# Performance work log

Measured on AMD Instinct MI355X. Metric: run time of the kernel, lower is better.

The kernel has to match this reference:

```python
import jax, jax.numpy as jnp
import numpy as np

B, N, C_FEAT = 2, 1024, 64
S, K, K_FP = 512, 32, 3
D_MODEL, N_HEAD = 128, 4
EPS_BN = 1e-5


def square_distance(src, dst):
    # src [B,N,3], dst [B,M,3] -> [B,N,M], same expansion as torch version
    d = -2.0 * jnp.einsum('bnc,bmc->bnm', src, dst)
    d = d + jnp.sum(src ** 2, -1)[:, :, None]
    d = d + jnp.sum(dst ** 2, -1)[:, None, :]
    return d


def gather_points(points, idx):
    # points [B,N,C], idx [B,...] int -> [B,...,C]  (index_points)
    return jax.vmap(lambda p, i: p[i])(points, idx)


def fps(xyz, n_samples):
    # furthest point sampling, deterministic start at index 0
    Bs, Np, _ = xyz.shape
    def step(carry, _):
        dist, far = carry
        centroid = jax.vmap(lambda p, i: p[i])(xyz, far)  # [B,3]
        d = jnp.sum((xyz - centroid[:, None, :]) ** 2, -1)
        dist = jnp.minimum(dist, d)
        new_far = jnp.argmax(dist, -1).astype(jnp.int32)
        return (dist, new_far), far
    init = (jnp.full((Bs, Np), 1e10, xyz.dtype), jnp.zeros((Bs,), jnp.int32))
    _, idxs = jax.lax.scan(step, init, None, length=n_samples)
    return idxs.T  # [B,S]


def knn(nsample, xyz, new_xyz):
    d = square_distance(new_xyz, xyz)
    _, idx = jax.lax.top_k(-d, nsample)
    return idx  # [B, n_query, nsample]


def setup_inputs() -> dict:
    key = jax.random.key(0)
    ks = jax.random.split(key, 12)
    Din = 2 * C_FEAT + 3  # 131 = 3 + 2*channels (PreExtraction in_channels)
    def lin(k, fan_in, shape):
        return (jax.random.normal(k, shape, jnp.float32) / np.sqrt(fan_in)).astype(jnp.float32)
    z = lambda n: jnp.zeros((n,), jnp.float32)
    return {
        'xyz': jax.random.normal(ks[0], (B, N, 3), jnp.float32),
        'feats': jax.random.normal(ks[1], (B, N, C_FEAT), jnp.float32),
        'affine_alpha': jnp.ones((1, 1, 1, C_FEAT + 3), jnp.float32),
        'affine_beta': jnp.zeros((1, 1, 1, C_FEAT + 3), jnp.float32),
        'W_t': lin(ks[2], Din, (Din, D_MODEL)), 'b_t': z(D_MODEL),
        'bn_g': jnp.ones((D_MODEL,), jnp.float32), 'bn_b': z(D_MODEL),
        'Wq': lin(ks[3], D_MODEL, (D_MODEL, D_MODEL)), 'bq': z(D_MODEL),
        'Wk': lin(ks[4], D_MODEL, (D_MODEL, D_MODEL)), 'bk': z(D_MODEL),
        'Wv': lin(ks[5], D_MODEL, (D_MODEL, D_MODEL)), 'bv': z(D_MODEL),
        'Wo': lin(ks[6], D_MODEL, (D_MODEL, D_MODEL)), 'bo': z(D_MODEL),
        'Wp1': lin(ks[7], 3, (3, D_MODEL)), 'bp1': z(D_MODEL),
        'Wp2': lin(ks[8], D_MODEL, (D_MODEL, N_HEAD)), 'bp2': z(N_HEAD),
    }


def reference(xyz, feats, affine_alpha, affine_beta, W_t, b_t, bn_g, bn_b,
              Wq, bq, Wk, bk, Wv, bv, Wo, bo, Wp1, bp1, Wp2, bp2):
    # ---- LocalGrouper (FPS + KNN + gather + center-normalize + affine) ----
    fps_idx = fps(xyz, S)                       # [B,S]
    new_xyz = gather_points(xyz, fps_idx)       # [B,S,3]
    anchor_feats = gather_points(feats, fps_idx)  # [B,S,C]
    idx = knn(K, xyz, new_xyz)                  # [B,S,K]
    grouped_xyz = gather_points(xyz, idx)       # [B,S,K,3]
    grouped_pts = gather_points(feats, idx)     # [B,S,K,C]
    grouped = jnp.concatenate([grouped_pts, grouped_xyz], -1)  # [B,S,K,C+3]
    mean = jnp.mean(grouped, axis=2, keepdims=True)
    std = jnp.std((grouped - mean).reshape(B, -1), axis=-1, ddof=1)[:, None, None, None]
    grouped = (grouped - mean) / (std + 1e-5)
    grouped = affine_alpha * grouped + affine_beta
    anchor_rep = jnp.broadcast_to(anchor_feats[:, :, None, :], (B, S, K, C_FEAT))
    new_points = jnp.concatenate([grouped, anchor_rep], -1)  # [B,S,K,2C+3]
    # ---- PreExtraction transfer (1x1 conv + BN(eval) + ReLU) + max over K ----
    y = jnp.einsum('bskd,do->bsko', new_points, W_t) + b_t
    y = y * (bn_g / jnp.sqrt(1.0 + EPS_BN)) + bn_b  # BN with running stats (0,1)
    y = jax.nn.relu(y)
    v_k = jnp.max(y, axis=2)                    # [B,S,D_MODEL]
    # ---- PointNetFeaturePropagation (KNN-3 inverse-distance interp) ----
    idx_fp = knn(K_FP, new_xyz, xyz)            # [B,N,3]
    sqrd = square_distance(xyz, new_xyz)        # [B,N,S]
    d_near = jnp.clip(jnp.take_along_axis(sqrd, idx_fp, axis=2), 1e-10, None)
    w = 1.0 / d_near
    w = w / jnp.sum(w, -1, keepdims=True)
    grouped_v = gather_points(v_k, idx_fp)      # [B,N,3,D]
    v_q = jnp.einsum('bnk,bnkc->bnc', w, grouped_v)  # [B,N,D]
    # ---- PointTransformerCrossAttention ----
    Dh = D_MODEL // N_HEAD
    qh = (v_q @ Wq + bq).reshape(B, N, N_HEAD, Dh)
    kh = (v_k @ Wk + bk).reshape(B, S, N_HEAD, Dh)
    vh = (v_k @ Wv + bv).reshape(B, S, N_HEAD, Dh)
    rel = xyz[:, :, None, :] - new_xyz[:, None, :, :]         # [B,N,S,3]
    rpe = jax.nn.relu(rel @ Wp1 + bp1) @ Wp2 + bp2            # [B,N,S,H]
    energy = jnp.einsum('bihd,bjhd->bhij', qh, kh) / jnp.sqrt(jnp.float32(Dh))
    attn = jax.nn.softmax(energy + rpe.transpose(0, 3, 1, 2), axis=-1)
    out = jnp.einsum('bhij,bjhd->bihd', attn, vh).reshape(B, N, D_MODEL)
    return out @ Wo + bo
```

## Files before the change

### kernel.cpp

```cpp
#include <hip/hip_runtime.h>
#include <math.h>

namespace {

constexpr int B  = 2;
constexpr int N  = 1024;
constexpr int CF = 64;
constexpr int S  = 512;
constexpr int K  = 32;
constexpr int DM = 128;
constexpr int NH = 4;
constexpr int DH = 32;
constexpr int GC = 67;
constexpr int DIN = 131;
constexpr int DPAD = 132;
constexpr int EPAD = 516;

typedef float f2 __attribute__((ext_vector_type(2)));

__device__ inline float max3f(float a, float b, float c) { return fmaxf(fmaxf(a, b), c); }
__device__ inline unsigned min3u(unsigned a, unsigned b, unsigned c) { return min(min(a, b), c); }

template <int CTRL>
__device__ inline float dpp_mov_f(float v) {
  return __int_as_float(__builtin_amdgcn_update_dpp(0, __float_as_int(v), CTRL, 0xF, 0xF, true));
}
template <int CTRL>
__device__ inline unsigned dpp_mov_self_u(unsigned v) {
  return (unsigned)__builtin_amdgcn_update_dpp((int)v, (int)v, CTRL, 0xF, 0xF, false);
}

__global__ void __launch_bounds__(64, 1)
fps_kernel(const float* __restrict__ xyz, int* __restrict__ fps_idx,
           float* __restrict__ new_xyz) {
  const int b = blockIdx.x;
  const int lane = threadIdx.x;
  __shared__ __align__(16) float4 pts4[N];
  __shared__ int farhist[S];
  for (int p = lane; p < N; p += 64) {
    pts4[p] = make_float4(xyz[b*N*3 + p*3+0], xyz[b*N*3 + p*3+1], xyz[b*N*3 + p*3+2], 0.0f);
  }
  __syncthreads();
  f2 X[8], Y[8], Z[8];
  float dist[16];
  #pragma unroll
  for (int j = 0; j < 8; ++j) {
    const float4 a = pts4[(2*j)*64 + lane];
    const float4 c = pts4[(2*j+1)*64 + lane];
    X[j] = f2{a.x, c.x}; Y[j] = f2{a.y, c.y}; Z[j] = f2{a.z, c.z};
  }
  #pragma unroll
  for (int k = 0; k < 16; ++k) dist[k] = 1e10f;
  int far = 0;
  for (int s = 0; s < S; ++s) {
    if (lane == 0) farhist[s] = far;
    const float4 c = pts4[far];
    const f2 cx = f2{c.x, c.x}, cy = f2{c.y, c.y}, cz = f2{c.z, c.z};
    #pragma unroll
    for (int j = 0; j < 8; ++j) {
      const f2 dx = X[j] - cx, dy = Y[j] - cy, dz = Z[j] - cz;
      const f2 q = dx*dx + dy*dy + dz*dz;
      dist[2*j]   = fminf(dist[2*j],   q.x);
      dist[2*j+1] = fminf(dist[2*j+1], q.y);
    }
    const float l0 = max3f(dist[0],  dist[1],  dist[2]);
    const float l1 = max3f(dist[3],  dist[4],  dist[5]);
    const float l2 = max3f(dist[6],  dist[7],  dist[8]);
    const float l3 = max3f(dist[9],  dist[10], dist[11]);
    const float l4 = max3f(dist[12], dist[13], dist[14]);
    float mv = fmaxf(max3f(l0, l1, l2), max3f(l3, l4, dist[15]));
    mv = fmaxf(mv, dpp_mov_f<0x111>(mv));
    mv = fmaxf(mv, dpp_mov_f<0x112>(mv));
    mv = fmaxf(mv, dpp_mov_f<0x114>(mv));
    mv = fmaxf(mv, dpp_mov_f<0x118>(mv));
    mv = fmaxf(mv, dpp_mov_f<0x142>(mv));
    mv = fmaxf(mv, dpp_mov_f<0x143>(mv));
    const float maxv = __int_as_float(__builtin_amdgcn_readlane(__float_as_int(mv), 63));
    unsigned cnd[16];
    #pragma unroll
    for (int k = 0; k < 16; ++k) {
      cnd[k] = (dist[k] == maxv) ? (unsigned)(k*64 + lane) : 0xFFFFFFFFu;
    }
    const unsigned u0 = min3u(cnd[0],  cnd[1],  cnd[2]);
    const unsigned u1 = min3u(cnd[3],  cnd[4],  cnd[5]);
    const unsigned u2 = min3u(cnd[6],  cnd[7],  cnd[8]);
    const unsigned u3 = min3u(cnd[9],  cnd[10], cnd[11]);
    const unsigned u4 = min3u(cnd[12], cnd[13], cnd[14]);
    unsigned cand = min(min3u(u0, u1, u2), min3u(u3, u4, cnd[15]));
    cand = min(cand, dpp_mov_self_u<0x111>(cand));
    cand = min(cand, dpp_mov_self_u<0x112>(cand));
    cand = min(cand, dpp_mov_self_u<0x114>(cand));
    cand = min(cand, dpp_mov_self_u<0x118>(cand));
    cand = min(cand, dpp_mov_self_u<0x142>(cand));
    cand = min(cand, dpp_mov_self_u<0x143>(cand));
    far = __builtin_amdgcn_readlane((int)cand, 63);
  }
  __syncthreads();
  for (int s = lane; s < S; s += 64) {
    const int f = farhist[s];
    const float4 c = pts4[f];
    fps_idx[b*S+s] = f;
    new_xyz[(b*S+s)*3+0] = c.x;
    new_xyz[(b*S+s)*3+1] = c.y;
    new_xyz[(b*S+s)*3+2] = c.z;
  }
}

__global__ void knn_kernel(const float* __restrict__ xyz, const float* __restrict__ feats,
                           const float* __restrict__ new_xyz, int* __restrict__ knn_idx,
                           float* __restrict__ mean_out, float2* __restrict__ partials) {
  const int b = blockIdx.y;
  const int tid = threadIdx.x;
  const int wave = tid >> 6, lane = tid & 63;
  const int s = blockIdx.x * 4 + wave;
  __shared__ float pts[N*3];
  __shared__ int sidx_s[4][K];
  for (int i = tid; i < N*3; i += 256) pts[i] = xyz[b*N*3 + i];
  __syncthreads();
  const float qx = new_xyz[(b*S+s)*3+0], qy = new_xyz[(b*S+s)*3+1], qz = new_xyz[(b*S+s)*3+2];
  const float qn = qx*qx + qy*qy + qz*qz;
  float d[16];
  #pragma unroll
  for (int j = 0; j < 16; ++j) {
    const int p = j*64 + lane;
    const float px = pts[p*3+0], py = pts[p*3+1], pz = pts[p*3+2];
    const float dot = qx*px + qy*py + qz*pz;
    const float pn  = px*px + py*py + pz*pz;
    d[j] = (-2.0f*dot + qn) + pn;
  }
  unsigned mask = 0xFFFFu;
  for (int k = 0; k < K; ++k) {
    float bv = INFINITY; int bj = 0;
    #pragma unroll
    for (int j = 0; j < 16; ++j) {
      if (((mask >> j) & 1u) && d[j] < bv) { bv = d[j]; bj = j; }
    }
    int bp = bj*64 + lane;
    #pragma unroll
    for (int m = 1; m < 64; m <<= 1) {
      const float ov = __shfl_xor(bv, m);
      const int   op = __shfl_xor(bp, m);
      if (ov < bv || (ov == bv && op < bp)) { bv = ov; bp = op; }
    }
    if (lane == 0) { knn_idx[(b*S+s)*K + k] = bp; sidx_s[wave][k] = bp; }
    if ((bp & 63) == lane) mask &= ~(1u << (bp >> 6));
  }
  const int bs = b*S + s;
  float ls = 0.0f, lsq = 0.0f;
  float v[K];
  {
    const int c = lane;
    float sum = 0.0f;
    #pragma unroll
    for (int k = 0; k < K; ++k) {
      const int p = sidx_s[wave][k];
      const float g = feats[(b*N+p)*CF + c];
      v[k] = g; sum += g;
    }
    const float mean = sum * (1.0f/K);
    mean_out[bs*GC + c] = mean;
    #pragma unroll
    for (int k = 0; k < K; ++k) {
      const float cc = v[k] - mean;
      ls += cc; lsq += cc*cc;
    }
  }
  if (lane < 3) {
    const int c = CF + lane;
    float sum = 0.0f;
    #pragma unroll
    for (int k = 0; k < K; ++k) {
      const int p = sidx_s[wave][k];
      const float g = xyz[(b*N+p)*3 + lane];
      v[k] = g; sum += g;
    }
    const float mean = sum * (1.0f/K);
    mean_out[bs*GC + c] = mean;
    #pragma unroll
    for (int k = 0; k < K; ++k) {
      const float cc = v[k] - mean;
      ls += cc; lsq += cc*cc;
    }
  }
  #pragma unroll
  for (int m = 1; m < 64; m <<= 1) { ls += __shfl_xor(ls, m); lsq += __shfl_xor(lsq, m); }
  if (lane == 0) partials[bs] = make_float2(ls, lsq);
}

__global__ void stats_kernel(const float2* __restrict__ partials, float* __restrict__ invstd) {
  const int b = blockIdx.x;
  const int lane = threadIdx.x;
  double su = 0.0, sq = 0.0;
  for (int i = lane; i < S; i += 64) {
    const float2 p = partials[b*S+i];
    su += (double)p.x; sq += (double)p.y;
  }
  #pragma unroll
  for (int m = 1; m < 64; m <<= 1) { su += __shfl_xor(su, m); sq += __shfl_xor(sq, m); }
  if (lane == 0) {
    const double nn = (double)S * K * GC;
    const double var = (sq - su*su/nn) / (nn - 1.0);
    invstd[b] = 1.0f / ((float)sqrt(var) + 1e-5f);
  }
}

__global__ void transfer_kernel(const float* __restrict__ feats, const float* __restrict__ xyz,
                                const int* __restrict__ knn_idx, const int* __restrict__ fps_idx,
                                const float* __restrict__ mean_in, const float* __restrict__ invstd,
                                const float* __restrict__ alpha, const float* __restrict__ beta,
                                const float* __restrict__ W_t, const float* __restrict__ b_t,
                                const float* __restrict__ bn_g, const float* __restrict__ bn_b,
                                const float* __restrict__ Wk, const float* __restrict__ bk,
                                const float* __restrict__ Wv, const float* __restrict__ bv,
                                float* __restrict__ v_k, float* __restrict__ kpb,
                                float* __restrict__ vpb) {
  const int bs = blockIdx.x;
  const int b = bs / S;
  const int t = threadIdx.x;
  __shared__ __align__(16) float np_s[K][DPAD];
  __shared__ float vrow[DM];
  __shared__ int sidx[K];
  __shared__ int sanchor;
  if (t < K) sidx[t] = knn_idx[bs*K + t];
  if (t == 0) sanchor = fps_idx[bs];
  __syncthreads();
  const float sinv = invstd[b];
  for (int k = 0; k < K; ++k) {
    const int p = sidx[k];
    for (int c = t; c < DPAD; c += 128) {
      float val = 0.0f;
      if (c < GC) {
        const float g = (c < CF) ? feats[(b*N+p)*CF + c] : xyz[(b*N+p)*3 + (c-CF)];
        val = (g - mean_in[bs*GC + c]) * sinv * alpha[c] + beta[c];
      } else if (c < DIN) {
        val = feats[(b*N+sanchor)*CF + (c - GC)];
      }
      np_s[k][c] = val;
    }
  }
  __syncthreads();
  float acc[K];
  const float bt = b_t[t];
  #pragma unroll
  for (int k = 0; k < K; ++k) acc[k] = bt;
  for (int d4 = 0; d4 < DPAD/4; ++d4) {
    const int d = d4*4;
    const float w0 = W_t[(d+0)*DM + t];
    const float w1 = W_t[(d+1)*DM + t];
    const float w2 = W_t[(d+2)*DM + t];
    const float w3 = (d+3 < DIN) ? W_t[(d+3)*DM + t] : 0.0f;
    #pragma unroll
    for (int k = 0; k < K; ++k) {
      const float4 f = *reinterpret_cast<const float4*>(&np_s[k][d]);
      acc[k] = acc[k] + f.x*w0 + f.y*w1 + f.z*w2 + f.w*w3;
    }
  }
  const float scale = bn_g[t] / sqrtf(1.0f + 1e-5f);
  const float shift = bn_b[t];
  float mx = -INFINITY;
  #pragma unroll
  for (int k = 0; k < K; ++k) {
    const float y = fmaxf(acc[k]*scale + shift, 0.0f);
    mx = fmaxf(mx, y);
  }
  v_k[bs*DM + t] = mx;
  vrow[t] = mx;
  __syncthreads();
  float acck = bk[t], accv = bv[t];
  for (int d = 0; d < DM; ++d) {
    const float f = vrow[d];
    acck += f * Wk[d*DM + t];
    accv += f * Wv[d*DM + t];
  }
  kpb[bs*DM + t] = acck;
  vpb[bs*DM + t] = accv;
}

__global__ void interp_kernel(const float* __restrict__ xyz, const float* __restrict__ new_xyz,
                              const float* __restrict__ v_k, const float* __restrict__ Wq,
                              const float* __restrict__ bq, float* __restrict__ qbuf) {
  const int b = blockIdx.y;
  const int tid = threadIdx.x;
  const int wave = tid >> 6, lane = tid & 63;
  const int n = blockIdx.x*4 + wave;
  __shared__ float pts[S*3];
  __shared__ float vqs[4][DM];
  for (int i = tid; i < S*3; i += 256) pts[i] = new_xyz[b*S*3 + i];
  __syncthreads();
  const float qx = xyz[(b*N+n)*3+0], qy = xyz[(b*N+n)*3+1], qz = xyz[(b*N+n)*3+2];
  const float qn = qx*qx + qy*qy + qz*qz;
  float d[8];
  #pragma unroll
  for (int j = 0; j < 8; ++j) {
    const int p = j*64 + lane;
    const float px = pts[p*3+0], py = pts[p*3+1], pz = pts[p*3+2];
    const float dot = qx*px + qy*py + qz*pz;
    const float pn  = px*px + py*py + pz*pz;
    d[j] = (-2.0f*dot + qn) + pn;
  }
  unsigned mask = 0xFFu;
  float sd[3]; int sp[3];
  #pragma unroll
  for (int k = 0; k < 3; ++k) {
    float bv = INFINITY; int bj = 0;
    #pragma unroll
    for (int j = 0; j < 8; ++j) {
      if (((mask >> j) & 1u) && d[j] < bv) { bv = d[j]; bj = j; }
    }
    int bp = bj*64 + lane;
    #pragma unroll
    for (int m = 1; m < 64; m <<= 1) {
      const float ov = __shfl_xor(bv, m);
      const int   op = __shfl_xor(bp, m);
      if (ov < bv || (ov == bv && op < bp)) { bv = ov; bp = op; }
    }
    sd[k] = bv; sp[k] = bp;
    if ((bp & 63) == lane) mask &= ~(1u << (bp >> 6));
  }
  float w0 = 1.0f / fmaxf(sd[0], 1e-10f);
  float w1 = 1.0f / fmaxf(sd[1], 1e-10f);
  float w2 = 1.0f / fmaxf(sd[2], 1e-10f);
  const float wsum = w0 + w1 + w2;
  w0 /= wsum; w1 /= wsum; w2 /= wsum;
  const float* vk0 = v_k + (b*S + sp[0])*DM;
  const float* vk1 = v_k + (b*S + sp[1])*DM;
  const float* vk2 = v_k + (b*S + sp[2])*DM;
  #pragma unroll
  for (int c = lane; c < DM; c += 64) {
    vqs[wave][c] = w0*vk0[c] + w1*vk1[c] + w2*vk2[c];
  }
  __syncthreads();
  const float* row = vqs[wave];
  #pragma unroll
  for (int half = 0; half < 2; ++half) {
    const int c = lane + half*64;
    float acc = bq[c];
    for (int d = 0; d < DM; ++d) acc += row[d] * Wq[d*DM + c];
    qbuf[(b*N+n)*DM + c] = acc;
  }
}

__global__ void attn_kernel(const float* __restrict__ xyz, const float* __restrict__ new_xyz,
                            const float* __restrict__ qb, const float* __restrict__ kp,
                            const float* __restrict__ vp, const float* __restrict__ Wp1,
                            const float* __restrict__ bp1, const float* __restrict__ Wp2,
                            const float* __restrict__ bp2, const float* __restrict__ Wo,
                            const float* __restrict__ bo, float* __restrict__ out) {
  const int bn = blockIdx.x;
  const int b = bn / N;
  const int t = threadIdx.x;
  __shared__ __align__(16) float e[NH][EPAD];
  __shared__ float qn_s[DM];
  __shared__ float oa[DM];
  __shared__ float ssum[NH];
  qn_s[t] = qb[bn*DM + t];
  __syncthreads();
  const float qx = xyz[bn*3+0], qy = xyz[bn*3+1], qz = xyz[bn*3+2];
  const float rs = 0.17677669529663687f;
  for (int j = t; j < S; j += 128) {
    const float px = new_xyz[(b*S+j)*3+0], py = new_xyz[(b*S+j)*3+1], pz = new_xyz[(b*S+j)*3+2];
    const float rx = qx-px, ry = qy-py, rz = qz-pz;
    float r0 = bp2[0], r1 = bp2[1], r2 = bp2[2], r3 = bp2[3];
    for (int m = 0; m < DM; ++m) {
      float hm = rx*Wp1[m] + ry*Wp1[DM+m] + rz*Wp1[2*DM+m] + bp1[m];
      hm = fmaxf(hm, 0.0f);
      r0 += hm*Wp2[m*NH+0]; r1 += hm*Wp2[m*NH+1];
      r2 += hm*Wp2[m*NH+2]; r3 += hm*Wp2[m*NH+3];
    }
    const float rpe[NH] = {r0, r1, r2, r3};
    #pragma unroll
    for (int h = 0; h < NH; ++h) {
      const float* kr = kp + (b*S+j)*DM + h*DH;
      const float* qr = qn_s + h*DH;
      float acc = 0.0f;
      #pragma unroll
      for (int dd = 0; dd < DH; ++dd) acc += qr[dd]*kr[dd];
      e[h][j] = acc*rs + rpe[h];
    }
  }
  __syncthreads();
  const int h = t >> 5, g = t & 31;
  float mx = -INFINITY;
  for (int j = g; j < S; j += 32) mx = fmaxf(mx, e[h][j]);
  #pragma unroll
  for (int m = 16; m >= 1; m >>= 1) mx = fmaxf(mx, __shfl_xor(mx, m));
  float sum = 0.0f;
  for (int j = g; j < S; j += 32) { const float ex = expf(e[h][j]-mx); e[h][j] = ex; sum += ex; }
  #pragma unroll
  for (int m = 16; m >= 1; m >>= 1) sum += __shfl_xor(sum, m);
  if (g == 0) ssum[h] = sum;
  __syncthreads();
  float acc = 0.0f;
  for (int j = 0; j < S; j += 4) {
    const float4 ev = *reinterpret_cast<const float4*>(&e[h][j]);
    acc += ev.x * vp[(b*S+j+0)*DM + t];
    acc += ev.y * vp[(b*S+j+1)*DM + t];
    acc += ev.z * vp[(b*S+j+2)*DM + t];
    acc += ev.w * vp[(b*S+j+3)*DM + t];
  }
  oa[t] = acc / ssum[h];
  __syncthreads();
  float facc = bo[t];
  for (int d = 0; d < DM; ++d) facc += oa[d] * Wo[d*DM + t];
  out[bn*DM + t] = facc;
}

}

extern "C" void kernel_launch(void* const* d_in, const int* in_sizes, int n_in,
                              void* d_out, int out_size, void* d_ws, size_t ws_size,
                              hipStream_t stream) {
  const float* xyz   = (const float*)d_in[0];
  const float* feats = (const float*)d_in[1];
  const float* alpha = (const float*)d_in[2];
  const float* beta  = (const float*)d_in[3];
  const float* W_t   = (const float*)d_in[4];
  const float* b_t   = (const float*)d_in[5];
  const float* bn_g  = (const float*)d_in[6];
  const float* bn_b  = (const float*)d_in[7];
  const float* Wq = (const float*)d_in[8];  const float* bq = (const float*)d_in[9];
  const float* Wk = (const float*)d_in[10]; const float* bk = (const float*)d_in[11];
  const float* Wv = (const float*)d_in[12]; const float* bv = (const float*)d_in[13];
  const float* Wo = (const float*)d_in[14]; const float* bo = (const float*)d_in[15];
  const float* Wp1= (const float*)d_in[16]; const float* bp1= (const float*)d_in[17];
  const float* Wp2= (const float*)d_in[18]; const float* bp2= (const float*)d_in[19];

  char* w = (char*)d_ws;
  int*    fps_i = (int*)   (w + 0);
  float*  nxyz  = (float*) (w + 4096);
  int*    knn_i = (int*)   (w + 16384);
  float*  meanb = (float*) (w + 147456);
  float2* part  = (float2*)(w + 421888);
  float*  invs  = (float*) (w + 430080);
  float*  vk    = (float*) (w + 430336);
  float*  qbuf  = (float*) (w + 2003200);
  float*  kpb   = (float*) (w + 3051776);
  float*  vpb   = (float*) (w + 3576064);
  float*  outf  = (float*)d_out;

  fps_kernel<<<B, 64, 0, stream>>>(xyz, fps_i, nxyz);
  knn_kernel<<<dim3(S/4, B), 256, 0, stream>>>(xyz, feats, nxyz, knn_i, meanb, part);
  stats_kernel<<<B, 64, 0, stream>>>(part, invs);
  transfer_kernel<<<B*S, 128, 0, stream>>>(feats, xyz, knn_i, fps_i, meanb, invs,
                                           alpha, beta, W_t, b_t, bn_g, bn_b,
                                           Wk, bk, Wv, bv, vk, kpb, vpb);
  interp_kernel<<<dim3(N/4, B), 256, 0, stream>>>(xyz, nxyz, vk, Wq, bq, qbuf);
  attn_kernel<<<B*N, 128, 0, stream>>>(xyz, nxyz, qbuf, kpb, vpb, Wp1, bp1, Wp2, bp2, Wo, bo, outf);
}
```

Before: 450.6 us.

## Widen attention blocks to 512 threads, splitting key loop and PV sum

The attention kernel now launches 512 threads per query point. Each thread computes the positional-encoding MLP and energies for exactly one key, where before each thread looped over four. The attn·V product is split into four key-range groups whose partial sums are reduced through shared memory, and key rows are read as float4. The aim is more parallelism per block and shorter serial loops, at the cost of extra syncs, idle threads during softmax and the output projection, and lower occupancy per block.

Result: faster. 423.6 us (-6.0%).

```diff
diff --git a/kernel.cpp b/kernel.cpp
--- a/kernel.cpp
+++ b/kernel.cpp
@@ -351,13 +351,14 @@
   const int t = threadIdx.x;
   __shared__ __align__(16) float e[NH][EPAD];
   __shared__ float qn_s[DM];
-  __shared__ float oa[DM];
+  __shared__ __align__(16) float oa4[4][DM];
   __shared__ float ssum[NH];
-  qn_s[t] = qb[bn*DM + t];
+  if (t < DM) qn_s[t] = qb[bn*DM + t];
   __syncthreads();
   const float qx = xyz[bn*3+0], qy = xyz[bn*3+1], qz = xyz[bn*3+2];
   const float rs = 0.17677669529663687f;
-  for (int j = t; j < S; j += 128) {
+  {
+    const int j = t;
     const float px = new_xyz[(b*S+j)*3+0], py = new_xyz[(b*S+j)*3+1], pz = new_xyz[(b*S+j)*3+2];
     const float rx = qx-px, ry = qy-py, rz = qz-pz;
     float r0 = bp2[0], r1 = bp2[1], r2 = bp2[2], r3 = bp2[3];
@@ -370,39 +371,58 @@
     const float rpe[NH] = {r0, r1, r2, r3};
     #pragma unroll
     for (int h = 0; h < NH; ++h) {
-      const float* kr = kp + (b*S+j)*DM + h*DH;
+      const float4* kr4 = reinterpret_cast<const float4*>(kp + (b*S+j)*DM + h*DH);
       const float* qr = qn_s + h*DH;
       float acc = 0.0f;
       #pragma unroll
-      for (int dd = 0; dd < DH; ++dd) acc += qr[dd]*kr[dd];
+      for (int dd = 0; dd < 8; ++dd) {
+        const float4 kv = kr4[dd];
+        acc += qr[dd*4+0]*kv.x + qr[dd*4+1]*kv.y + qr[dd*4+2]*kv.z + qr[dd*4+3]*kv.w;
+      }
       e[h][j] = acc*rs + rpe[h];
     }
   }
   __syncthreads();
-  const int h = t >> 5, g = t & 31;
-  float mx = -INFINITY;
-  for (int j = g; j < S; j += 32) mx = fmaxf(mx, e[h][j]);
-  #pragma unroll
-  for (int m = 16; m >= 1; m >>= 1) mx = fmaxf(mx, __shfl_xor(mx, m));
-  float sum = 0.0f;
-  for (int j = g; j < S; j += 32) { const float ex = expf(e[h][j]-mx); e[h][j] = ex; sum += ex; }
-  #pragma unroll
-  for (int m = 16; m >= 1; m >>= 1) sum += __shfl_xor(sum, m);
-  if (g == 0) ssum[h] = sum;
-  __syncthreads();
-  float acc = 0.0f;
-  for (int j = 0; j < S; j += 4) {
-    const float4 ev = *reinterpret_cast<const float4*>(&e[h][j]);
-    acc += ev.x * vp[(b*S+j+0)*DM + t];
-    acc += ev.y * vp[(b*S+j+1)*DM + t];
-    acc += ev.z * vp[(b*S+j+2)*DM + t];
-    acc += ev.w * vp[(b*S+j+3)*DM + t];
-  }
-  oa[t] = acc / ssum[h];
-  __syncthreads();
-  float facc = bo[t];
-  for (int d = 0; d < DM; ++d) facc += oa[d] * Wo[d*DM + t];
-  out[bn*DM + t] = facc;
+  if (t < 128) {
+    const int h = t >> 5, g = t & 31;
+    float mx = -INFINITY;
+    for (int j = g; j < S; j += 32) mx = fmaxf(mx, e[h][j]);
+    #pragma unroll
+    for (int m = 16; m >= 1; m >>= 1) mx = fmaxf(mx, __shfl_xor(mx, m));
+    float sum = 0.0f;
+    for (int j = g; j < S; j += 32) { const float ex = expf(e[h][j]-mx); e[h][j] = ex; sum += ex; }
+    #pragma unroll
+    for (int m = 16; m >= 1; m >>= 1) sum += __shfl_xor(sum, m);
+    if (g == 0) ssum[h] = sum;
+  }
+  __syncthreads();
+  {
+    const int grp = t >> 7;
+    const int tt = t & 127;
+    const int h = tt >> 5;
+    float acc = 0.0f;
+    const int j0 = grp*128;
+    for (int j = j0; j < j0 + 128; j += 4) {
+      const float4 ev = *reinterpret_cast<const float4*>(&e[h][j]);
+      acc += ev.x * vp[(b*S+j+0)*DM + tt];
+      acc += ev.y * vp[(b*S+j+1)*DM + tt];
+      acc += ev.z * vp[(b*S+j+2)*DM + tt];
+      acc += ev.w * vp[(b*S+j+3)*DM + tt];
+    }
+    oa4[grp][tt] = acc;
+  }
+  __syncthreads();
+  if (t < 128) {
+    const int h = t >> 5;
+    const float total = ((oa4[0][t] + oa4[1][t]) + oa4[2][t]) + oa4[3][t];
+    oa4[0][t] = total / ssum[h];
+  }
+  __syncthreads();
+  if (t < 128) {
+    float facc = bo[t];
+    for (int d = 0; d < DM; ++d) facc += oa4[0][d] * Wo[d*DM + t];
+    out[bn*DM + t] = facc;
+  }
 }
 
 }
@@ -445,5 +465,5 @@
                                            alpha, beta, W_t, b_t, bn_g, bn_b,
                                            Wk, bk, Wv, bv, vk, kpb, vpb);
   interp_kernel<<<dim3(N/4, B), 256, 0, stream>>>(xyz, nxyz, vk, Wq, bq, qbuf);
-  attn_kernel<<<B*N, 128, 0, stream>>>(xyz, nxyz, qbuf, kpb, vpb, Wp1, bp1, Wp2, bp2, Wo, bo, outf);
-}
+  attn_kernel<<<B*N, 512, 0, stream>>>(xyz, nxyz, qbuf, kpb, vpb, Wp1, bp1, Wp2, bp2, Wo, bo, outf);
+}
```
